# Kernel tuning notes

Measured on AMD Instinct MI355X. Metric: run time of the kernel, lower is better.

## Reference

```python
import jax, jax.numpy as jnp
import numpy as np

NUM_ITERATIONS = 5
USE_SYMMETRIC_FINAL = True


def setup_inputs() -> dict:
    key = jax.random.key(0)
    k1, _ = jax.random.split(key)
    log_scores = jax.random.normal(k1, (4, 16, 1024, 1024), dtype=jnp.float32)
    tau = jnp.float32(1.0)
    return {"log_scores": log_scores, "tau": tau}


def reference(log_scores, tau):
    # tau clamped to min 0.1 as in torch .clamp(min=0.1)
    tau_c = jnp.maximum(tau, jnp.float32(0.1))
    ls = log_scores / tau_c
    # Sinkhorn iterations: alternate row / column logsumexp normalization.
    for _ in range(NUM_ITERATIONS):
        ls = ls - jax.nn.logsumexp(ls, axis=-1, keepdims=True)  # row normalize
        ls = ls - jax.nn.logsumexp(ls, axis=-2, keepdims=True)  # col normalize
    if USE_SYMMETRIC_FINAL:
        ls = ls - jax.nn.logsumexp(ls, axis=-1, keepdims=True)
        ls_col = ls - jax.nn.logsumexp(ls, axis=-2, keepdims=True)
        ls = 0.5 * (ls + ls_col)
    return jnp.exp(ls)
```

## Files before the change

kernel.cpp:

```cpp
#include <hip/hip_runtime.h>
#include <hip/hip_fp16.h>


#define NROWS 1024
#define NCOLS 1024
#define NMAT 64
#define MATELEMS (NROWS * NCOLS)
#define NSTRIPE 16
#define SCOLS 64
#define SH8 8

struct __align__(16) H8 { __half2 h[4]; };

__device__ __forceinline__ float wave_sum(float v) {
#pragma unroll
  for (int o = 32; o > 0; o >>= 1) v += __shfl_xor(v, o, 64);
  return v;
}

__global__ __launch_bounds__(256) void convert_row(
    const float* __restrict__ x, __half* __restrict__ t,
    float* __restrict__ S, const float* __restrict__ tau) {
  const float it = 1.0f / fmaxf(tau[0], 0.1f);
  const int row = blockIdx.x * 4 + (threadIdx.x >> 6);
  const int lane = threadIdx.x & 63;
  const float4* xr = (const float4*)(x + (size_t)row * NCOLS);
  H8* tr = (H8*)(t + (size_t)row * NCOLS);
  float s = 0.0f;
#pragma unroll
  for (int k = 0; k < 2; ++k) {
    const int f4 = k * 128 + lane * 2;
    float4 a = xr[f4];
    float4 b = xr[f4 + 1];
    a.x *= it; a.y *= it; a.z *= it; a.w *= it;
    b.x *= it; b.y *= it; b.z *= it; b.w *= it;
    H8 o;
    o.h[0] = __floats2half2_rn(a.x, a.y);
    o.h[1] = __floats2half2_rn(a.z, a.w);
    o.h[2] = __floats2half2_rn(b.x, b.y);
    o.h[3] = __floats2half2_rn(b.z, b.w);
    tr[k * 64 + lane] = o;
    s += __expf(a.x) + __expf(a.y) + __expf(a.z) + __expf(a.w) +
         __expf(b.x) + __expf(b.y) + __expf(b.z) + __expf(b.w);
  }
  s = wave_sum(s);
  if (lane == 0) S[row] = s;
}

template <int FINAL>
__global__ __launch_bounds__(1024) void fused_col(
    const __half* __restrict__ t, const float* __restrict__ Pin, const int ns,
    const float* __restrict__ cin, float* __restrict__ cout,
    float* __restrict__ Pout, float* __restrict__ out) {
  const int mat = blockIdx.x >> 4;
  const int sb = blockIdx.x & 15;
  const int tid = threadIdx.x;
  const __half* tb = t + (size_t)mat * MATELEMS + sb * SCOLS;

  __shared__ H8 tile[NROWS * SH8];
  __shared__ float r_lds[NROWS];
  __shared__ float wred[16][SCOLS];
  __shared__ float c_lds[SCOLS];

  {
    const float* pb = Pin + (size_t)mat * ns * NROWS + tid;
    float acc = 0.0f;
    for (int s2 = 0; s2 < ns; ++s2) acc += pb[s2 * NROWS];
    r_lds[tid] = __logf(acc);
  }
  __syncthreads();

  const int c8 = tid & 7;
  const int rowg = tid >> 3;
  float s[8];
#pragma unroll
  for (int j = 0; j < 8; ++j) s[j] = 0.0f;
#pragma unroll
  for (int ch = 0; ch < 8; ++ch) {
    const int row = ch * 128 + rowg;
    H8 v = ((const H8*)(tb + (size_t)row * NCOLS))[c8];
    tile[row * SH8 + (c8 ^ (row & 7))] = v;
    const float ri = r_lds[row];
    float2 f0 = __half22float2(v.h[0]);
    float2 f1 = __half22float2(v.h[1]);
    float2 f2 = __half22float2(v.h[2]);
    float2 f3 = __half22float2(v.h[3]);
    s[0] += __expf(f0.x - ri); s[1] += __expf(f0.y - ri);
    s[2] += __expf(f1.x - ri); s[3] += __expf(f1.y - ri);
    s[4] += __expf(f2.x - ri); s[5] += __expf(f2.y - ri);
    s[6] += __expf(f3.x - ri); s[7] += __expf(f3.y - ri);
  }
#pragma unroll
  for (int j = 0; j < 8; ++j) {
    s[j] += __shfl_xor(s[j], 8, 64);
    s[j] += __shfl_xor(s[j], 16, 64);
    s[j] += __shfl_xor(s[j], 32, 64);
  }
  if ((tid & 63) < 8) {
    const int wv = tid >> 6;
#pragma unroll
    for (int j = 0; j < 8; ++j) wred[wv][c8 * 8 + j] = s[j];
  }
  __syncthreads();
  if (tid < SCOLS) {
    float acc = 0.0f;
#pragma unroll
    for (int w = 0; w < 16; ++w) acc += wred[w][tid];
    const float lse = __logf(acc);
    if (FINAL) {
      c_lds[tid] = 0.5f * (lse + cin[mat * NCOLS + sb * SCOLS + tid]);
    } else {
      c_lds[tid] = lse;
      cout[mat * NCOLS + sb * SCOLS + tid] = lse;
    }
  }
  __syncthreads();

  if (!FINAL) {
    const int row = tid;
    const int sw = row & 7;
    float rp0 = 0.0f, rp1 = 0.0f;
#pragma unroll
    for (int g = 0; g < 8; ++g) {
      H8 v = tile[row * SH8 + (g ^ sw)];
      float2 f0 = __half22float2(v.h[0]);
      float2 f1 = __half22float2(v.h[1]);
      float2 f2 = __half22float2(v.h[2]);
      float2 f3 = __half22float2(v.h[3]);
      const float* cj = &c_lds[g * 8];
      rp0 += __expf(f0.x - cj[0]) + __expf(f0.y - cj[1]) +
             __expf(f1.x - cj[2]) + __expf(f1.y - cj[3]);
      rp1 += __expf(f2.x - cj[4]) + __expf(f2.y - cj[5]) +
             __expf(f3.x - cj[6]) + __expf(f3.y - cj[7]);
    }
    Pout[((size_t)mat * NSTRIPE + sb) * NROWS + row] = rp0 + rp1;
  } else {
    const int colh = tid & 7;
    const int rg = tid >> 3;
    float h[8];
#pragma unroll
    for (int j = 0; j < 8; ++j) h[j] = c_lds[colh * 8 + j];
    float* ob = out + (size_t)mat * MATELEMS + sb * SCOLS;
#pragma unroll
    for (int ch = 0; ch < 8; ++ch) {
      const int row = ch * 128 + rg;
      H8 v = tile[row * SH8 + (colh ^ (row & 7))];
      const float ri = r_lds[row];
      float2 f0 = __half22float2(v.h[0]);
      float2 f1 = __half22float2(v.h[1]);
      float2 f2 = __half22float2(v.h[2]);
      float2 f3 = __half22float2(v.h[3]);
      float4 o0, o1;
      o0.x = __expf(f0.x - ri - h[0]);
      o0.y = __expf(f0.y - ri - h[1]);
      o0.z = __expf(f1.x - ri - h[2]);
      o0.w = __expf(f1.y - ri - h[3]);
      o1.x = __expf(f2.x - ri - h[4]);
      o1.y = __expf(f2.y - ri - h[5]);
      o1.z = __expf(f3.x - ri - h[6]);
      o1.w = __expf(f3.y - ri - h[7]);
      float4* op = (float4*)(ob + (size_t)row * NCOLS) + colh * 2;
      op[0] = o0;
      op[1] = o1;
    }
  }
}

extern "C" void kernel_launch(void* const* d_in, const int* in_sizes, int n_in,
                              void* d_out, int out_size, void* d_ws,
                              size_t ws_size, hipStream_t stream) {
  const float* x = (const float*)d_in[0];
  const float* tau = (const float*)d_in[1];
  float* out = (float*)d_out;

  __half* t = (__half*)d_ws;
  float* S1 = (float*)((char*)d_ws + (size_t)NMAT * MATELEMS * sizeof(__half));
  float* PA = S1 + NMAT * NROWS;
  float* PB = PA + NMAT * NSTRIPE * NROWS;
  float* c = PB + NMAT * NSTRIPE * NROWS;

  const int row_grid = NMAT * NROWS / 4;
  const int f_grid = NMAT * NSTRIPE;

  convert_row<<<row_grid, 256, 0, stream>>>(x, t, S1, tau);
  fused_col<0><<<f_grid, 1024, 0, stream>>>(t, S1, 1, nullptr, c, PA, nullptr);
  fused_col<0><<<f_grid, 1024, 0, stream>>>(t, PA, NSTRIPE, nullptr, c, PB, nullptr);
  fused_col<0><<<f_grid, 1024, 0, stream>>>(t, PB, NSTRIPE, nullptr, c, PA, nullptr);
  fused_col<0><<<f_grid, 1024, 0, stream>>>(t, PA, NSTRIPE, nullptr, c, PB, nullptr);
  fused_col<0><<<f_grid, 1024, 0, stream>>>(t, PB, NSTRIPE, nullptr, c, PA, nullptr);
  fused_col<1><<<f_grid, 1024, 0, stream>>>(t, PA, NSTRIPE, c, nullptr, nullptr, out);
}
```

Baseline: 745.8 us.

## Run Sinkhorn in linear domain with stored exp values and reciprocal scalings

The intermediate matrix now holds exp(x/tau) in fp16 instead of log-scores, so every normalization pass multiplies by row and column reciprocal scalings rather than evaluating exp and log per element. The symmetric final average becomes a geometric mean through 1/sqrt of the two column sums. This takes most transcendental work out of the column and row passes. In exchange it risks fp16 overflow or underflow when tau is small, which a fixed shift only partly guards against.

```diff
diff --git a/kernel.cpp b/kernel.cpp
--- a/kernel.cpp
+++ b/kernel.cpp
@@ -22,6 +22,7 @@
     const float* __restrict__ x, __half* __restrict__ t,
     float* __restrict__ S, const float* __restrict__ tau) {
   const float it = 1.0f / fmaxf(tau[0], 0.1f);
+  const float sh = fmaxf(0.0f, 6.0f * it - 10.0f);
   const int row = blockIdx.x * 4 + (threadIdx.x >> 6);
   const int lane = threadIdx.x & 63;
   const float4* xr = (const float4*)(x + (size_t)row * NCOLS);
@@ -30,18 +31,23 @@
 #pragma unroll
   for (int k = 0; k < 2; ++k) {
     const int f4 = k * 128 + lane * 2;
-    float4 a = xr[f4];
-    float4 b = xr[f4 + 1];
-    a.x *= it; a.y *= it; a.z *= it; a.w *= it;
-    b.x *= it; b.y *= it; b.z *= it; b.w *= it;
+    float4 va = xr[f4];
+    float4 vb = xr[f4 + 1];
+    float e0 = __expf(va.x * it - sh);
+    float e1 = __expf(va.y * it - sh);
+    float e2 = __expf(va.z * it - sh);
+    float e3 = __expf(va.w * it - sh);
+    float e4 = __expf(vb.x * it - sh);
+    float e5 = __expf(vb.y * it - sh);
+    float e6 = __expf(vb.z * it - sh);
+    float e7 = __expf(vb.w * it - sh);
     H8 o;
-    o.h[0] = __floats2half2_rn(a.x, a.y);
-    o.h[1] = __floats2half2_rn(a.z, a.w);
-    o.h[2] = __floats2half2_rn(b.x, b.y);
-    o.h[3] = __floats2half2_rn(b.z, b.w);
+    o.h[0] = __floats2half2_rn(e0, e1);
+    o.h[1] = __floats2half2_rn(e2, e3);
+    o.h[2] = __floats2half2_rn(e4, e5);
+    o.h[3] = __floats2half2_rn(e6, e7);
     tr[k * 64 + lane] = o;
-    s += __expf(a.x) + __expf(a.y) + __expf(a.z) + __expf(a.w) +
-         __expf(b.x) + __expf(b.y) + __expf(b.z) + __expf(b.w);
+    s += e0 + e1 + e2 + e3 + e4 + e5 + e6 + e7;
   }
   s = wave_sum(s);
   if (lane == 0) S[row] = s;
@@ -66,7 +72,7 @@
     const float* pb = Pin + (size_t)mat * ns * NROWS + tid;
     float acc = 0.0f;
     for (int s2 = 0; s2 < ns; ++s2) acc += pb[s2 * NROWS];
-    r_lds[tid] = __logf(acc);
+    r_lds[tid] = 1.0f / acc;
   }
   __syncthreads();
 
@@ -80,15 +86,15 @@
     const int row = ch * 128 + rowg;
     H8 v = ((const H8*)(tb + (size_t)row * NCOLS))[c8];
     tile[row * SH8 + (c8 ^ (row & 7))] = v;
-    const float ri = r_lds[row];
+    const float ui = r_lds[row];
     float2 f0 = __half22float2(v.h[0]);
     float2 f1 = __half22float2(v.h[1]);
     float2 f2 = __half22float2(v.h[2]);
     float2 f3 = __half22float2(v.h[3]);
-    s[0] += __expf(f0.x - ri); s[1] += __expf(f0.y - ri);
-    s[2] += __expf(f1.x - ri); s[3] += __expf(f1.y - ri);
-    s[4] += __expf(f2.x - ri); s[5] += __expf(f2.y - ri);
-    s[6] += __expf(f3.x - ri); s[7] += __expf(f3.y - ri);
+    s[0] += f0.x * ui; s[1] += f0.y * ui;
+    s[2] += f1.x * ui; s[3] += f1.y * ui;
+    s[4] += f2.x * ui; s[5] += f2.y * ui;
+    s[6] += f3.x * ui; s[7] += f3.y * ui;
   }
 #pragma unroll
   for (int j = 0; j < 8; ++j) {
@@ -106,12 +112,11 @@
     float acc = 0.0f;
 #pragma unroll
     for (int w = 0; w < 16; ++w) acc += wred[w][tid];
-    const float lse = __logf(acc);
     if (FINAL) {
-      c_lds[tid] = 0.5f * (lse + cin[mat * NCOLS + sb * SCOLS + tid]);
+      c_lds[tid] = 1.0f / sqrtf(acc * cin[mat * NCOLS + sb * SCOLS + tid]);
     } else {
-      c_lds[tid] = lse;
-      cout[mat * NCOLS + sb * SCOLS + tid] = lse;
+      cout[mat * NCOLS + sb * SCOLS + tid] = acc;
+      c_lds[tid] = 1.0f / acc;
     }
   }
   __syncthreads();
@@ -128,10 +133,8 @@
       float2 f2 = __half22float2(v.h[2]);
       float2 f3 = __half22float2(v.h[3]);
       const float* cj = &c_lds[g * 8];
-      rp0 += __expf(f0.x - cj[0]) + __expf(f0.y - cj[1]) +
-             __expf(f1.x - cj[2]) + __expf(f1.y - cj[3]);
-      rp1 += __expf(f2.x - cj[4]) + __expf(f2.y - cj[5]) +
-             __expf(f3.x - cj[6]) + __expf(f3.y - cj[7]);
+      rp0 += f0.x * cj[0] + f0.y * cj[1] + f1.x * cj[2] + f1.y * cj[3];
+      rp1 += f2.x * cj[4] + f2.y * cj[5] + f3.x * cj[6] + f3.y * cj[7];
     }
     Pout[((size_t)mat * NSTRIPE + sb) * NROWS + row] = rp0 + rp1;
   } else {
@@ -145,20 +148,20 @@
     for (int ch = 0; ch < 8; ++ch) {
       const int row = ch * 128 + rg;
       H8 v = tile[row * SH8 + (colh ^ (row & 7))];
-      const float ri = r_lds[row];
+      const float ui = r_lds[row];
       float2 f0 = __half22float2(v.h[0]);
       float2 f1 = __half22float2(v.h[1]);
       float2 f2 = __half22float2(v.h[2]);
       float2 f3 = __half22float2(v.h[3]);
       float4 o0, o1;
-      o0.x = __expf(f0.x - ri - h[0]);
-      o0.y = __expf(f0.y - ri - h[1]);
-      o0.z = __expf(f1.x - ri - h[2]);
-      o0.w = __expf(f1.y - ri - h[3]);
-      o1.x = __expf(f2.x - ri - h[4]);
-      o1.y = __expf(f2.y - ri - h[5]);
-      o1.z = __expf(f3.x - ri - h[6]);
-      o1.w = __expf(f3.y - ri - h[7]);
+      o0.x = f0.x * ui * h[0];
+      o0.y = f0.y * ui * h[1];
+      o0.z = f1.x * ui * h[2];
+      o0.w = f1.y * ui * h[3];
+      o1.x = f2.x * ui * h[4];
+      o1.y = f2.y * ui * h[5];
+      o1.z = f3.x * ui * h[6];
+      o1.w = f3.y * ui * h[7];
       float4* op = (float4*)(ob + (size_t)row * NCOLS) + colh * 2;
       op[0] = o0;
       op[1] = o1;
```

Result: faster. 709.9 us (-4.8%).
